# Kernel optimization log

Measured on AMD Instinct MI355X. Metric: run time of the kernel, lower is better.

## Reference

```python
import jax, jax.numpy as jnp
import numpy as np

D_MODEL = 5120
NUM_HEADS = 128
HEAD_DIM = D_MODEL // NUM_HEADS  # 40
LATENT = 1536


def setup_inputs() -> dict:
    key = jax.random.key(0)
    ks = jax.random.split(key, 9)
    B, S = 2, 1024
    scale = 0.02
    return {
        "x": jax.random.normal(ks[0], (B, S, D_MODEL), dtype=jnp.float32),
        "Wq": jax.random.normal(ks[1], (D_MODEL, D_MODEL), dtype=jnp.float32) * scale,
        "bq": jnp.zeros((D_MODEL,), dtype=jnp.float32),
        "Wc": jax.random.normal(ks[2], (D_MODEL, LATENT), dtype=jnp.float32) * scale,
        "bc": jnp.zeros((LATENT,), dtype=jnp.float32),
        "Wk": jax.random.normal(ks[3], (LATENT, D_MODEL), dtype=jnp.float32) * scale,
        "bk": jnp.zeros((D_MODEL,), dtype=jnp.float32),
        "Wv": jax.random.normal(ks[4], (LATENT, D_MODEL), dtype=jnp.float32) * scale,
        "bv": jnp.zeros((D_MODEL,), dtype=jnp.float32),
    }


def reference(x, Wq, bq, Wc, bc, Wk, bk, Wv, bv):
    B, S, _ = x.shape
    H, Dh = NUM_HEADS, HEAD_DIM
    # projections
    q = x @ Wq + bq                     # [B,S,D]
    kv_latent = x @ Wc + bc             # [B,S,L]
    k = kv_latent @ Wk + bk             # [B,S,D]
    v = kv_latent @ Wv + bv             # [B,S,D]
    # split heads -> [B,H,S,Dh]
    q = q.reshape(B, S, H, Dh).transpose(0, 2, 1, 3)
    k = k.reshape(B, S, H, Dh).transpose(0, 2, 1, 3)
    v = v.reshape(B, S, H, Dh).transpose(0, 2, 1, 3)
    scores = jnp.einsum("bhqd,bhkd->bhqk", q, k) / jnp.sqrt(jnp.float32(Dh))
    attn = jax.nn.softmax(scores, axis=-1)
    out = jnp.einsum("bhqk,bhkd->bhqd", attn, v)  # [B,H,S,Dh]
    return out.transpose(0, 2, 1, 3).reshape(B, S, H * Dh)
```

## Files before the change

kernel.cpp:

```cpp
#include <hip/hip_runtime.h>
#include <hip/hip_bf16.h>

typedef __attribute__((ext_vector_type(8))) __bf16 bf16x8;
typedef __attribute__((ext_vector_type(4))) __bf16 bf16x4;
typedef __attribute__((ext_vector_type(4))) float f32x4;

#define MFMA16(a, b, c) __builtin_amdgcn_mfma_f32_16x16x32_bf16((a), (b), (c), 0, 0, 0)

#if __has_builtin(__builtin_amdgcn_exp2f)
#define EXP2F(x) __builtin_amdgcn_exp2f(x)
#else
#define EXP2F(x) exp2f(x)
#endif

#define GLDS16(g, l)                                                             \
    __builtin_amdgcn_global_load_lds((const __attribute__((address_space(1))) void*)(g), \
                                     (__attribute__((address_space(3))) void*)(l), 16, 0, 0)

#define BARRIER()                          \
    do {                                   \
        asm volatile("" ::: "memory");     \
        __builtin_amdgcn_s_barrier();      \
        asm volatile("" ::: "memory");     \
    } while (0)

#define WAIT_LGKM0() asm volatile("s_waitcnt lgkmcnt(0)" ::: "memory")
#define VM6 asm volatile("s_waitcnt vmcnt(6)" ::: "memory")
#define VM8 asm volatile("s_waitcnt vmcnt(8)" ::: "memory")
#define VM0 asm volatile("s_waitcnt vmcnt(0)" ::: "memory")
#define VMNONE ((void)0)
#define KEEP(x) x
#define DROP(x)

static __device__ __forceinline__ unsigned short cvt_bf(float f) {
    return __builtin_bit_cast(unsigned short, (__bf16)f);
}

static __device__ __forceinline__ bf16x8 bf8_zero() {
    uint4 z = make_uint4(0, 0, 0, 0);
    return __builtin_bit_cast(bf16x8, z);
}

__global__ __launch_bounds__(256) void prep(const float* __restrict__ X,
                                            const float* __restrict__ Wq,
                                            const float* __restrict__ Wc,
                                            const float* __restrict__ Wk,
                                            const float* __restrict__ Wv,
                                            unsigned short* __restrict__ Xb,
                                            unsigned short* __restrict__ dqc,
                                            unsigned short* __restrict__ dkv) {
    const int D = 5120, L = 1536;
    int b = blockIdx.x, t = threadIdx.x;
    if (b < 5120) {
        int i = (b * 256 + t) * 8;
        float4 f0 = *(const float4*)(X + i);
        float4 f1 = *(const float4*)(X + i + 4);
        unsigned short o[8];
        o[0] = cvt_bf(f0.x); o[1] = cvt_bf(f0.y); o[2] = cvt_bf(f0.z); o[3] = cvt_bf(f0.w);
        o[4] = cvt_bf(f1.x); o[5] = cvt_bf(f1.y); o[6] = cvt_bf(f1.z); o[7] = cvt_bf(f1.w);
        *(uint4*)(Xb + i) = *(const uint4*)o;
        return;
    }
    int b2 = b - 5120;
    const float* W;
    unsigned short* WT;
    int K, N;
    if (b2 < 6400) { W = Wq; WT = dqc; K = D; N = D; }
    else if (b2 < 8320) { b2 -= 6400; W = Wc; WT = dqc + (size_t)D * D; K = D; N = L; }
    else if (b2 < 10240) { b2 -= 8320; W = Wk; WT = dkv; K = L; N = D; }
    else { b2 -= 10240; W = Wv; WT = dkv + (size_t)D * L; K = L; N = D; }
    int nx = N / 64;
    int n0 = (b2 % nx) * 64, k0 = (b2 / nx) * 64;

    __shared__ unsigned short tile[64][65];
    int c4 = (t & 15) * 4, r16 = t >> 4;
#pragma unroll
    for (int it = 0; it < 4; ++it) {
        int r = r16 + it * 16;
        float4 f = *(const float4*)&W[(size_t)(k0 + r) * N + n0 + c4];
        tile[r][c4 + 0] = cvt_bf(f.x);
        tile[r][c4 + 1] = cvt_bf(f.y);
        tile[r][c4 + 2] = cvt_bf(f.z);
        tile[r][c4 + 3] = cvt_bf(f.w);
    }
    __syncthreads();
    int n = t >> 2, kc = (t & 3) * 16;
    unsigned short o[16];
#pragma unroll
    for (int j = 0; j < 16; ++j) o[j] = tile[kc + j][n];
    unsigned short* dst = &WT[(size_t)(n0 + n) * K + k0 + kc];
    *(uint4*)dst = *(const uint4*)o;
    *(uint4*)(dst + 8) = *(const uint4*)(o + 8);
}

#define STAGE_A(S, H, KT)                                                              \
    do {                                                                               \
        GLDS16(aS[H][0] + (size_t)(KT) * 64, &Abuf[S][(H) * 8192 + wid * 512]);        \
        GLDS16(aS[H][1] + (size_t)(KT) * 64, &Abuf[S][(H) * 8192 + 4096 + wid * 512]); \
    } while (0)
#define STAGE_B(S, H, KT)                                                              \
    do {                                                                               \
        GLDS16(bS[H][0] + (size_t)(KT) * 64, &Bbuf[S][(H) * 8192 + wid * 512]);        \
        GLDS16(bS[H][1] + (size_t)(KT) * 64, &Bbuf[S][(H) * 8192 + 4096 + wid * 512]); \
    } while (0)

#define LDA_HALF(S, QM)                                                                   \
    do {                                                                                  \
        _Pragma("unroll") for (int mi = 0; mi < 4; ++mi)                                  \
            _Pragma("unroll") for (int kh = 0; kh < 2; ++kh)                              \
                af[mi][kh] =                                                              \
                    *(const bf16x8*)&Abuf[S][((QM) * 8192 + aoff + mi * 1024) ^ (kh * 32)]; \
    } while (0)
#define LDB_HALF(S, QN, BF)                                                               \
    do {                                                                                  \
        _Pragma("unroll") for (int ni = 0; ni < 2; ++ni)                                  \
            _Pragma("unroll") for (int kh = 0; kh < 2; ++kh)                              \
                BF[ni][kh] =                                                              \
                    *(const bf16x8*)&Bbuf[S][((QN) * 8192 + boff + ni * 1024) ^ (kh * 32)]; \
    } while (0)

#define MMAQ(QM, QN, BF)                                                                \
    do {                                                                                \
        _Pragma("unroll") for (int mi = 0; mi < 4; ++mi)                                \
            _Pragma("unroll") for (int ni = 0; ni < 2; ++ni)                            \
                _Pragma("unroll") for (int kh = 0; kh < 2; ++kh)                        \
                    acc[(QM) * 4 + mi][(QN) * 2 + ni] =                                 \
                        MFMA16(af[mi][kh], BF[ni][kh], acc[(QM) * 4 + mi][(QN) * 2 + ni]); \
    } while (0)

#define KTILE_V2(S, T, STG1, STG2, VMOP, RDNEXT)       \
    {                                                  \
        const int s_ = (S);                            \
        LDB_HALF(s_, 1, bf1);                          \
        STG1(STAGE_B(s_ ^ 1, 0, (T) + 1);)             \
        __builtin_amdgcn_s_setprio(1);                 \
        MMAQ(0, 0, bf0);                               \
        __builtin_amdgcn_s_setprio(0);                 \
        WAIT_LGKM0();                                  \
        BARRIER();                                     \
        STG2(STAGE_A(s_, 0, (T) + 2);                  \
             STAGE_B(s_, 1, (T) + 2);)                 \
        __builtin_amdgcn_s_setprio(1);                 \
        MMAQ(0, 1, bf1);                               \
        __builtin_amdgcn_s_setprio(0);                 \
        LDA_HALF(s_, 1);                               \
        __builtin_amdgcn_s_setprio(1);                 \
        MMAQ(1, 1, bf1);                               \
        __builtin_amdgcn_s_setprio(0);                 \
        WAIT_LGKM0();                                  \
        BARRIER();                                     \
        STG2(STAGE_A(s_, 1, (T) + 2);)                 \
        __builtin_amdgcn_s_setprio(1);                 \
        MMAQ(1, 0, bf0);                               \
        __builtin_amdgcn_s_setprio(0);                 \
        VMOP;                                          \
        BARRIER();                                     \
        RDNEXT(LDA_HALF(s_ ^ 1, 0); LDB_HALF(s_ ^ 1, 0, bf0);) \
    }

__global__ __launch_bounds__(512, 2) void gemm256(const unsigned short* __restrict__ A, int lda,
                                                  const unsigned short* __restrict__ BT, int ldb,
                                                  const float* __restrict__ bias0,
                                                  const float* __restrict__ bias1, int nsplit,
                                                  unsigned short* __restrict__ C, int ldc,
                                                  int K, float s0, float s1, int gx) {
    __shared__ __align__(16) unsigned short Abuf[2][16384];
    __shared__ __align__(16) unsigned short Bbuf[2][16384];

    int nwg = gridDim.x, orig = blockIdx.x;
    int cpx = nwg >> 3;
    int wgid = (orig & 7) * cpx + (orig >> 3);
    int tm = wgid / gx, tn = wgid % gx;
    int m0 = tm * 256, n0 = tn * 256;

    int tid = threadIdx.x, lane = tid & 63, wid = tid >> 6;
    int wm = wid >> 2, wn = wid & 3;
    int lrow = lane & 15, lkg = lane >> 4;

    int t5 = tid >> 3;
    int cole = ((tid & 7) ^ ((tid >> 3) & 7)) << 3;
    const unsigned short* aS[2][2];
    const unsigned short* bS[2][2];
#pragma unroll
    for (int H = 0; H < 2; ++H)
#pragma unroll
        for (int c = 0; c < 2; ++c) {
            int rA = (c << 7) | (H << 6) | t5;
            int rB = (((c << 1) | (t5 >> 5)) << 6) | (H << 5) | (t5 & 31);
            aS[H][c] = A + (size_t)(m0 + rA) * lda + cole;
            bS[H][c] = BT + (size_t)(n0 + rB) * ldb + cole;
        }

    int xorc = (lkg * 8) ^ ((lrow & 7) << 3);
    int aoff = wm * 4096 + lrow * 64 + xorc;
    int boff = wn * 2048 + lrow * 64 + xorc;

    f32x4 acc[8][4];
#pragma unroll
    for (int i = 0; i < 8; ++i)
#pragma unroll
        for (int j = 0; j < 4; ++j) acc[i][j] = (f32x4){0.f, 0.f, 0.f, 0.f};
    bf16x8 af[4][2], bf0[2][2], bf1[2][2];

    const int nkt = K >> 6;

    STAGE_A(0, 0, 0); STAGE_A(0, 1, 0); STAGE_B(0, 0, 0); STAGE_B(0, 1, 0);
    STAGE_A(1, 0, 1); STAGE_B(1, 1, 1); STAGE_A(1, 1, 1);
    VM6;
    BARRIER();
    LDA_HALF(0, 0);
    LDB_HALF(0, 0, bf0);

    int t = 0;
    for (; t + 2 < nkt; ++t) KTILE_V2(t & 1, t, KEEP, KEEP, VM6, KEEP);
    KTILE_V2(t & 1, t, KEEP, DROP, VM0, KEEP);
    ++t;
    KTILE_V2(t & 1, t, DROP, DROP, VMNONE, DROP);

#pragma unroll
    for (int ni = 0; ni < 4; ++ni) {
        int col = n0 + wn * 64 + ni * 16 + lrow;
        float bval = (col < nsplit) ? bias0[col] : bias1[col - nsplit];
        float scl = (col < nsplit) ? s0 : s1;
#pragma unroll
        for (int mi = 0; mi < 8; ++mi) {
            int row = m0 + wm * 128 + mi * 16 + lkg * 4;
#pragma unroll
            for (int j = 0; j < 4; ++j)
                C[(size_t)(row + j) * ldc + col] = cvt_bf((acc[mi][ni][j] + bval) * scl);
        }
    }
}

#define STG128(S, KT)                                                                  \
    do {                                                                               \
        _Pragma("unroll") for (int i_ = 0; i_ < 4; ++i_)                               \
            GLDS16(Ag + (size_t)(i_ * 32) * lda + (size_t)(KT) * 64,                   \
                   &Abuf[S][i_ * 2048 + wid * 512]);                                   \
        _Pragma("unroll") for (int i_ = 0; i_ < 4; ++i_)                               \
            GLDS16(Bg + (size_t)(i_ * 32) * ldb + (size_t)(KT) * 64,                   \
                   &Bbuf[S][i_ * 2048 + wid * 512]);                                   \
    } while (0)

__global__ __launch_bounds__(256, 4) void gemm128(const unsigned short* __restrict__ A, int lda,
                                                  const unsigned short* __restrict__ BT, int ldb,
                                                  const float* __restrict__ bias0,
                                                  const float* __restrict__ bias1, int nsplit,
                                                  unsigned short* __restrict__ C, int ldc,
                                                  int K, float s0, float s1, int gy) {
    __shared__ __align__(16) unsigned short Abuf[2][8192];
    __shared__ __align__(16) unsigned short Bbuf[2][8192];

    int b = blockIdx.x;
    int tm = b % gy, tn = b / gy;
    int m0 = tm * 128, n0 = tn * 128;
    int tid = threadIdx.x, lane = tid & 63, wid = tid >> 6;
    int wm = wid >> 1, wn = wid & 1;
    int lrow = lane & 15, lkg = lane >> 4;

    int srow = tid >> 3;
    int cole = ((tid & 7) ^ ((tid >> 3) & 7)) << 3;
    const unsigned short* Ag = A + (size_t)(m0 + srow) * lda + cole;
    const unsigned short* Bg = BT + (size_t)(n0 + srow) * ldb + cole;

    int xorc8 = (lrow & 7) << 3;
    int aoff = (wm * 64 + lrow) * 64;
    int boff = (wn * 64 + lrow) * 64;

    f32x4 acc[4][4];
#pragma unroll
    for (int i = 0; i < 4; ++i)
#pragma unroll
        for (int j = 0; j < 4; ++j) acc[i][j] = (f32x4){0.f, 0.f, 0.f, 0.f};

    const int nkt = K >> 6;
    STG128(0, 0);
    for (int t = 0; t < nkt; ++t) {
        const int cur = t & 1;
        if (t + 1 < nkt) {
            STG128(cur ^ 1, t + 1);
            VM8;
        } else {
            VM0;
        }
        BARRIER();
        bf16x8 af[4][2], bv[4][2];
#pragma unroll
        for (int mi = 0; mi < 4; ++mi)
#pragma unroll
            for (int kh = 0; kh < 2; ++kh)
                af[mi][kh] = *(const bf16x8*)&Abuf[cur][aoff + mi * 1024 + (((kh * 4 + lkg) << 3) ^ xorc8)];
#pragma unroll
        for (int ni = 0; ni < 4; ++ni)
#pragma unroll
            for (int kh = 0; kh < 2; ++kh)
                bv[ni][kh] = *(const bf16x8*)&Bbuf[cur][boff + ni * 1024 + (((kh * 4 + lkg) << 3) ^ xorc8)];
        __builtin_amdgcn_s_setprio(1);
#pragma unroll
        for (int mi = 0; mi < 4; ++mi)
#pragma unroll
            for (int ni = 0; ni < 4; ++ni)
#pragma unroll
                for (int kh = 0; kh < 2; ++kh)
                    acc[mi][ni] = MFMA16(af[mi][kh], bv[ni][kh], acc[mi][ni]);
        __builtin_amdgcn_s_setprio(0);
        BARRIER();
    }

#pragma unroll
    for (int ni = 0; ni < 4; ++ni) {
        int col = n0 + wn * 64 + ni * 16 + lrow;
        float bval = (col < nsplit) ? bias0[col] : bias1[col - nsplit];
        float scl = (col < nsplit) ? s0 : s1;
#pragma unroll
        for (int mi = 0; mi < 4; ++mi) {
            int row = m0 + wm * 64 + mi * 16 + lkg * 4;
#pragma unroll
            for (int j = 0; j < 4; ++j)
                C[(size_t)(row + j) * ldc + col] = cvt_bf((acc[mi][ni][j] + bval) * scl);
        }
    }
}

__global__ __launch_bounds__(256) void attn(const unsigned short* __restrict__ q, int ldq,
                                            const unsigned short* __restrict__ k, int ldk,
                                            const unsigned short* __restrict__ v, int ldv,
                                            float* __restrict__ out) {
    const int S = 1024, D = 5120, Dh = 40;
    int b = blockIdx.z, h = blockIdx.y, qt = blockIdx.x;
    int t = threadIdx.x, lane = t & 63, wid = t >> 6;
    int lrow = lane & 15, lkg = lane >> 4;

    __shared__ __align__(16) unsigned short Ks[64 * 72];
    __shared__ __align__(16) unsigned short Vs[64 * 72];
    __shared__ __align__(16) unsigned short Ps[4][16 * 72];

    const size_t qbase = ((size_t)b * S) * ldq + (size_t)h * Dh;
    int q0 = qt * 64 + wid * 16;

    bf16x8 qf0, qf1;
    {
        const unsigned short* qp = q + qbase + (size_t)(q0 + lrow) * ldq;
        qf0 = *(const bf16x8*)(qp + lkg * 8);
        qf1 = (lkg == 0) ? *(const bf16x8*)(qp + 32) : bf8_zero();
    }

    int rrK = t >> 3, ccK = t & 7;
    int rrV = t & 63, ccV = t >> 6;
    const unsigned short* kp = k + ((size_t)b * S) * ldk + (size_t)h * Dh +
                               (size_t)rrK * ldk + ccK * 8;
    const unsigned short* vp = v + ((size_t)b * S) * ldv + (size_t)h * Dh +
                               (size_t)rrV * ldv + ccV * 8;
    const size_t kstep = (size_t)64 * ldk, vstep = (size_t)64 * ldv;

    uint4 kv0, kv1, vv0, vv1;
    kv0 = kv1 = vv0 = vv1 = make_uint4(0, 0, 0, 0);
    if (ccK < 5) { kv0 = *(const uint4*)kp; kv1 = *(const uint4*)(kp + 32 * ldk); }
    vv0 = *(const uint4*)vp;
    if (ccV == 0) vv1 = *(const uint4*)(vp + 32);
    kp += kstep; vp += vstep;

    f32x4 acc[3];
#pragma unroll
    for (int nb = 0; nb < 3; ++nb) acc[nb] = (f32x4){0.f, 0.f, 0.f, 0.f};
    float mrun = -INFINITY, lrun = 0.f;

    for (int kt = 0; kt < 16; ++kt) {
        __syncthreads();
        uint4 w0 = (ccK < 5) ? kv0 : make_uint4(0, 0, 0, 0);
        uint4 w1 = (ccK < 5) ? kv1 : make_uint4(0, 0, 0, 0);
        *(uint4*)&Ks[rrK * 72 + ccK * 8] = w0;
        *(uint4*)&Ks[(rrK + 32) * 72 + ccK * 8] = w1;
        {
            const unsigned short* pv = (const unsigned short*)&vv0;
#pragma unroll
            for (int j = 0; j < 8; ++j) Vs[(ccV * 8 + j) * 72 + rrV] = pv[j];
            if (ccV < 2) {
                uint4 z = (ccV == 0) ? vv1 : make_uint4(0, 0, 0, 0);
                const unsigned short* pz = (const unsigned short*)&z;
#pragma unroll
                for (int j = 0; j < 8; ++j) Vs[((ccV + 4) * 8 + j) * 72 + rrV] = pz[j];
            }
        }
        __syncthreads();
        if (kt + 1 < 16) {
            if (ccK < 5) { kv0 = *(const uint4*)kp; kv1 = *(const uint4*)(kp + 32 * ldk); }
            vv0 = *(const uint4*)vp;
            if (ccV == 0) vv1 = *(const uint4*)(vp + 32);
            kp += kstep; vp += vstep;
        }

        f32x4 sf[4];
        __builtin_amdgcn_s_setprio(1);
#pragma unroll
        for (int nb = 0; nb < 4; ++nb) {
            sf[nb] = (f32x4){0.f, 0.f, 0.f, 0.f};
            bf16x8 kf0 = *(const bf16x8*)&Ks[(nb * 16 + lrow) * 72 + lkg * 8];
            bf16x8 kf1 = *(const bf16x8*)&Ks[(nb * 16 + lrow) * 72 + 32 + lkg * 8];
            sf[nb] = MFMA16(kf0, qf0, sf[nb]);
            sf[nb] = MFMA16(kf1, qf1, sf[nb]);
        }
        __builtin_amdgcn_s_setprio(0);

        float tm = sf[0][0];
#pragma unroll
        for (int nb = 0; nb < 4; ++nb)
#pragma unroll
            for (int i = 0; i < 4; ++i) tm = fmaxf(tm, sf[nb][i]);
        tm = fmaxf(tm, __shfl_xor(tm, 16));
        tm = fmaxf(tm, __shfl_xor(tm, 32));

        float mn = mrun, al = 1.0f;
        bool resc = !__all(tm <= mrun + 11.0f);
        if (resc) {
            mn = fmaxf(mrun, tm);
            al = EXP2F(mrun - mn);
            mrun = mn;
        }
        float rs = 0.f;
#pragma unroll
        for (int nb = 0; nb < 4; ++nb) {
            bf16x4 pk;
#pragma unroll
            for (int i = 0; i < 4; ++i) {
                float p = EXP2F(sf[nb][i] - mn);
                rs += p;
                pk[i] = (__bf16)p;
            }
            *(bf16x4*)&Ps[wid][lrow * 72 + nb * 16 + lkg * 4] = pk;
        }
        rs += __shfl_xor(rs, 16);
        rs += __shfl_xor(rs, 32);
        lrun = lrun * al + rs;

        if (resc) {
            float alr[4];
#pragma unroll
            for (int i = 0; i < 4; ++i) alr[i] = __shfl(al, lkg * 4 + i);
#pragma unroll
            for (int nb = 0; nb < 3; ++nb)
#pragma unroll
                for (int i = 0; i < 4; ++i) acc[nb][i] *= alr[i];
        }

        __builtin_amdgcn_s_setprio(1);
#pragma unroll
        for (int kk = 0; kk < 2; ++kk) {
            bf16x8 pf = *(const bf16x8*)&Ps[wid][lrow * 72 + kk * 32 + lkg * 8];
#pragma unroll
            for (int nb = 0; nb < 3; ++nb) {
                bf16x8 vf = *(const bf16x8*)&Vs[(nb * 16 + lrow) * 72 + kk * 32 + lkg * 8];
                acc[nb] = MFMA16(pf, vf, acc[nb]);
            }
        }
        __builtin_amdgcn_s_setprio(0);
    }

    float lr[4];
#pragma unroll
    for (int i = 0; i < 4; ++i) lr[i] = __shfl(lrun, lkg * 4 + i);
#pragma unroll
    for (int i = 0; i < 4; ++i) {
        float inv = 1.0f / lr[i];
        int s = q0 + lkg * 4 + i;
#pragma unroll
        for (int nb = 0; nb < 3; ++nb) {
            int d = nb * 16 + lrow;
            if (d < Dh) out[((size_t)(b * S + s)) * D + h * Dh + d] = acc[nb][i] * inv;
        }
    }
}

extern "C" void kernel_launch(void* const* d_in, const int* in_sizes, int n_in,
                              void* d_out, int out_size, void* d_ws, size_t ws_size,
                              hipStream_t stream) {
    const int M = 2048, D = 5120, L = 1536, NQ = D + L , NKV = 2 * D ;
    const float* x  = (const float*)d_in[0];
    const float* Wq = (const float*)d_in[1];
    const float* bq = (const float*)d_in[2];
    const float* Wc = (const float*)d_in[3];
    const float* bc = (const float*)d_in[4];
    const float* Wk = (const float*)d_in[5];
    const float* bk = (const float*)d_in[6];
    const float* Wv = (const float*)d_in[7];
    const float* bv = (const float*)d_in[8];
    float* out = (float*)d_out;

    unsigned short* ws = (unsigned short*)d_ws;
    size_t off = 0;
    unsigned short* xb    = ws + off; off += (size_t)M * D;
    unsigned short* WqcT  = ws + off; off += (size_t)NQ * D;
    unsigned short* WkvT  = ws + off; off += (size_t)NKV * L;
    unsigned short* qkvb  = ws + off; off += (size_t)M * NQ;
    unsigned short* kvout = ws + off; off += (size_t)M * NKV;

    prep<<<17280, 256, 0, stream>>>(x, Wq, Wc, Wk, Wv, xb, WqcT, WkvT);

    const float qscale = 1.4426950408889634f / 6.324555320336759f;

    gemm256<<<dim3((NQ / 256) * (M / 256)), 512, 0, stream>>>(xb, D, WqcT, D, bq, bc, D,
                                                              qkvb, NQ, D, qscale, 1.0f,
                                                              NQ / 256);
    gemm128<<<dim3((NKV / 128) * (M / 128)), 256, 0, stream>>>(qkvb + D, NQ, WkvT, L, bk, bv, D,
                                                               kvout, NKV, L, 1.0f, 1.0f,
                                                               M / 128);

    attn<<<dim3(1024 / 64, 128, 2), 256, 0, stream>>>(qkvb, NQ, kvout, NKV, kvout + D, NKV, out);
}
```

Before: 466.0 us.

## Load GEMM B operand directly to registers and pre-transpose V for attention

The KV-projection GEMM now stages only the A tile through LDS and loads B fragments straight from global memory into registers, double-buffered two k-tiles ahead. This cuts LDS traffic and halves LDS use per block. A new vtrans kernel transposes V into a [D, tokens] buffer so the attention kernel can write V tiles to shared memory with vector stores instead of scalar scatter-transposes. The cost is an extra kernel launch plus a full round trip of V through memory, and B loads that now run uncoalesced across lanes.

```diff
diff --git a/kernel.cpp b/kernel.cpp
--- a/kernel.cpp
+++ b/kernel.cpp
@@ -26,7 +26,7 @@
 
 #define WAIT_LGKM0() asm volatile("s_waitcnt lgkmcnt(0)" ::: "memory")
 #define VM6 asm volatile("s_waitcnt vmcnt(6)" ::: "memory")
-#define VM8 asm volatile("s_waitcnt vmcnt(8)" ::: "memory")
+#define VM12 asm volatile("s_waitcnt vmcnt(12)" ::: "memory")
 #define VM0 asm volatile("s_waitcnt vmcnt(0)" ::: "memory")
 #define VMNONE ((void)0)
 #define KEEP(x) x
@@ -91,6 +91,28 @@
     unsigned short* dst = &WT[(size_t)(n0 + n) * K + k0 + kc];
     *(uint4*)dst = *(const uint4*)o;
     *(uint4*)(dst + 8) = *(const uint4*)(o + 8);
+}
+
+__global__ __launch_bounds__(256) void vtrans(const unsigned short* __restrict__ V, int ldv,
+                                              unsigned short* __restrict__ VT) {
+    int d0 = blockIdx.x * 64, s0 = blockIdx.y * 64;
+    __shared__ __align__(16) unsigned short tile[64][72];
+    int t = threadIdx.x;
+    int r = t >> 3, c8 = (t & 7) * 8;
+#pragma unroll
+    for (int p = 0; p < 2; ++p) {
+        uint4 u = *(const uint4*)&V[(size_t)(s0 + r + p * 32) * ldv + d0 + c8];
+        *(uint4*)&tile[r + p * 32][c8] = u;
+    }
+    __syncthreads();
+#pragma unroll
+    for (int p = 0; p < 2; ++p) {
+        int dr = (t >> 3) + p * 32, cc = (t & 7) * 8;
+        unsigned short o[8];
+#pragma unroll
+        for (int j = 0; j < 8; ++j) o[j] = tile[cc + j][dr];
+        *(uint4*)&VT[(size_t)(d0 + dr) * 2048 + s0 + cc] = *(const uint4*)o;
+    }
 }
 
 #define STAGE_A(S, H, KT)                                                              \
@@ -232,24 +254,46 @@
     }
 }
 
-#define STG128(S, KT)                                                                  \
+#define STGA128(P, T)                                                                  \
     do {                                                                               \
         _Pragma("unroll") for (int i_ = 0; i_ < 4; ++i_)                               \
-            GLDS16(Ag + (size_t)(i_ * 32) * lda + (size_t)(KT) * 64,                   \
-                   &Abuf[S][i_ * 2048 + wid * 512]);                                   \
-        _Pragma("unroll") for (int i_ = 0; i_ < 4; ++i_)                               \
-            GLDS16(Bg + (size_t)(i_ * 32) * ldb + (size_t)(KT) * 64,                   \
-                   &Bbuf[S][i_ * 2048 + wid * 512]);                                   \
-    } while (0)
-
-__global__ __launch_bounds__(256, 4) void gemm128(const unsigned short* __restrict__ A, int lda,
-                                                  const unsigned short* __restrict__ BT, int ldb,
-                                                  const float* __restrict__ bias0,
-                                                  const float* __restrict__ bias1, int nsplit,
-                                                  unsigned short* __restrict__ C, int ldc,
-                                                  int K, float s0, float s1, int gy) {
+            GLDS16(Ag + (size_t)(i_ * 32) * lda + (size_t)(T) * 64,                    \
+                   &Abuf[P][i_ * 2048 + wid * 512]);                                   \
+    } while (0)
+#define LDBQ(BV, T)                                                                    \
+    do {                                                                               \
+        _Pragma("unroll") for (int ni = 0; ni < 4; ++ni)                               \
+            _Pragma("unroll") for (int kh = 0; kh < 2; ++kh)                           \
+                BV[ni][kh] = *(const bf16x8*)(Bg[ni] + (size_t)(T) * 64 + kh * 32);    \
+    } while (0)
+
+#define ITERB(BV, P, T, STG_, LDB2_, VMOP)                                             \
+    {                                                                                  \
+        STG_(STGA128((P) ^ 1, (T) + 1);)                                               \
+        VMOP;                                                                          \
+        BARRIER();                                                                     \
+        bf16x8 af[4][2];                                                               \
+        _Pragma("unroll") for (int mi = 0; mi < 4; ++mi)                               \
+            _Pragma("unroll") for (int kh = 0; kh < 2; ++kh)                           \
+                af[mi][kh] = *(const bf16x8*)&Abuf[P][aoff + mi * 1024 +               \
+                                                      (((kh * 4 + lkg) << 3) ^ xorc8)]; \
+        __builtin_amdgcn_s_setprio(1);                                                 \
+        _Pragma("unroll") for (int mi = 0; mi < 4; ++mi)                               \
+            _Pragma("unroll") for (int ni = 0; ni < 4; ++ni)                           \
+                _Pragma("unroll") for (int kh = 0; kh < 2; ++kh)                       \
+                    acc[mi][ni] = MFMA16(af[mi][kh], BV[ni][kh], acc[mi][ni]);         \
+        __builtin_amdgcn_s_setprio(0);                                                 \
+        LDB2_(LDBQ(BV, (T) + 2);)                                                      \
+        BARRIER();                                                                     \
+    }
+
+__global__ __launch_bounds__(256, 4) void gemm128b(const unsigned short* __restrict__ A, int lda,
+                                                   const unsigned short* __restrict__ BT, int ldb,
+                                                   const float* __restrict__ bias0,
+                                                   const float* __restrict__ bias1, int nsplit,
+                                                   unsigned short* __restrict__ C, int ldc,
+                                                   int K, int gy) {
     __shared__ __align__(16) unsigned short Abuf[2][8192];
-    __shared__ __align__(16) unsigned short Bbuf[2][8192];
 
     int b = blockIdx.x;
     int tm = b % gy, tn = b / gy;
@@ -261,70 +305,52 @@
     int srow = tid >> 3;
     int cole = ((tid & 7) ^ ((tid >> 3) & 7)) << 3;
     const unsigned short* Ag = A + (size_t)(m0 + srow) * lda + cole;
-    const unsigned short* Bg = BT + (size_t)(n0 + srow) * ldb + cole;
+    const unsigned short* Bg[4];
+#pragma unroll
+    for (int ni = 0; ni < 4; ++ni)
+        Bg[ni] = BT + (size_t)(n0 + wn * 64 + ni * 16 + lrow) * ldb + lkg * 8;
 
     int xorc8 = (lrow & 7) << 3;
     int aoff = (wm * 64 + lrow) * 64;
-    int boff = (wn * 64 + lrow) * 64;
 
     f32x4 acc[4][4];
 #pragma unroll
     for (int i = 0; i < 4; ++i)
 #pragma unroll
         for (int j = 0; j < 4; ++j) acc[i][j] = (f32x4){0.f, 0.f, 0.f, 0.f};
+    bf16x8 bv0[4][2], bv1[4][2];
 
     const int nkt = K >> 6;
-    STG128(0, 0);
-    for (int t = 0; t < nkt; ++t) {
-        const int cur = t & 1;
-        if (t + 1 < nkt) {
-            STG128(cur ^ 1, t + 1);
-            VM8;
-        } else {
-            VM0;
-        }
-        BARRIER();
-        bf16x8 af[4][2], bv[4][2];
-#pragma unroll
-        for (int mi = 0; mi < 4; ++mi)
-#pragma unroll
-            for (int kh = 0; kh < 2; ++kh)
-                af[mi][kh] = *(const bf16x8*)&Abuf[cur][aoff + mi * 1024 + (((kh * 4 + lkg) << 3) ^ xorc8)];
-#pragma unroll
-        for (int ni = 0; ni < 4; ++ni)
-#pragma unroll
-            for (int kh = 0; kh < 2; ++kh)
-                bv[ni][kh] = *(const bf16x8*)&Bbuf[cur][boff + ni * 1024 + (((kh * 4 + lkg) << 3) ^ xorc8)];
-        __builtin_amdgcn_s_setprio(1);
-#pragma unroll
-        for (int mi = 0; mi < 4; ++mi)
-#pragma unroll
-            for (int ni = 0; ni < 4; ++ni)
-#pragma unroll
-                for (int kh = 0; kh < 2; ++kh)
-                    acc[mi][ni] = MFMA16(af[mi][kh], bv[ni][kh], acc[mi][ni]);
-        __builtin_amdgcn_s_setprio(0);
-        BARRIER();
-    }
+
+    LDBQ(bv0, 0);
+    STGA128(0, 0);
+    LDBQ(bv1, 1);
+
+    int T = 0;
+    for (; T + 2 < nkt; T += 2) {
+        ITERB(bv0, 0, T, KEEP, KEEP, VM12);
+        ITERB(bv1, 1, T + 1, KEEP, KEEP, VM12);
+    }
+    ITERB(bv0, 0, T, KEEP, DROP, VM12);
+    ITERB(bv1, 1, T + 1, DROP, DROP, VM0);
 
 #pragma unroll
     for (int ni = 0; ni < 4; ++ni) {
         int col = n0 + wn * 64 + ni * 16 + lrow;
         float bval = (col < nsplit) ? bias0[col] : bias1[col - nsplit];
-        float scl = (col < nsplit) ? s0 : s1;
 #pragma unroll
         for (int mi = 0; mi < 4; ++mi) {
             int row = m0 + wm * 64 + mi * 16 + lkg * 4;
 #pragma unroll
             for (int j = 0; j < 4; ++j)
-                C[(size_t)(row + j) * ldc + col] = cvt_bf((acc[mi][ni][j] + bval) * scl);
+                C[(size_t)(row + j) * ldc + col] = cvt_bf(acc[mi][ni][j] + bval);
         }
     }
 }
 
 __global__ __launch_bounds__(256) void attn(const unsigned short* __restrict__ q, int ldq,
                                             const unsigned short* __restrict__ k, int ldk,
-                                            const unsigned short* __restrict__ v, int ldv,
+                                            const unsigned short* __restrict__ vT,
                                             float* __restrict__ out) {
     const int S = 1024, D = 5120, Dh = 40;
     int b = blockIdx.z, h = blockIdx.y, qt = blockIdx.x;
@@ -332,11 +358,13 @@
     int lrow = lane & 15, lkg = lane >> 4;
 
     __shared__ __align__(16) unsigned short Ks[64 * 72];
-    __shared__ __align__(16) unsigned short Vs[64 * 72];
+    __shared__ __align__(16) unsigned short Vs[48 * 72];
     __shared__ __align__(16) unsigned short Ps[4][16 * 72];
 
     const size_t qbase = ((size_t)b * S) * ldq + (size_t)h * Dh;
     int q0 = qt * 64 + wid * 16;
+
+    for (int z = t; z < 8 * 72; z += 256) Vs[40 * 72 + z] = 0;
 
     bf16x8 qf0, qf1;
     {
@@ -346,19 +374,19 @@
     }
 
     int rrK = t >> 3, ccK = t & 7;
-    int rrV = t & 63, ccV = t >> 6;
+    int dV = t >> 3, cV = t & 7;
     const unsigned short* kp = k + ((size_t)b * S) * ldk + (size_t)h * Dh +
                                (size_t)rrK * ldk + ccK * 8;
-    const unsigned short* vp = v + ((size_t)b * S) * ldv + (size_t)h * Dh +
-                               (size_t)rrV * ldv + ccV * 8;
-    const size_t kstep = (size_t)64 * ldk, vstep = (size_t)64 * ldv;
-
-    uint4 kv0, kv1, vv0, vv1;
-    kv0 = kv1 = vv0 = vv1 = make_uint4(0, 0, 0, 0);
+    const unsigned short* vp = vT + (size_t)(h * Dh + dV) * 2048 + b * S + cV * 8;
+    const unsigned short* vp2 = vT + (size_t)(h * Dh + 32 + dV) * 2048 + b * S + cV * 8;
+    const size_t kstep = (size_t)64 * ldk;
+
+    uint4 kv0, kv1, va0, va1;
+    kv0 = kv1 = va0 = va1 = make_uint4(0, 0, 0, 0);
     if (ccK < 5) { kv0 = *(const uint4*)kp; kv1 = *(const uint4*)(kp + 32 * ldk); }
-    vv0 = *(const uint4*)vp;
-    if (ccV == 0) vv1 = *(const uint4*)(vp + 32);
-    kp += kstep; vp += vstep;
+    va0 = *(const uint4*)vp;
+    if (t < 64) va1 = *(const uint4*)vp2;
+    kp += kstep; vp += 64; vp2 += 64;
 
     f32x4 acc[3];
 #pragma unroll
@@ -371,23 +399,14 @@
         uint4 w1 = (ccK < 5) ? kv1 : make_uint4(0, 0, 0, 0);
         *(uint4*)&Ks[rrK * 72 + ccK * 8] = w0;
         *(uint4*)&Ks[(rrK + 32) * 72 + ccK * 8] = w1;
-        {
-            const unsigned short* pv = (const unsigned short*)&vv0;
-#pragma unroll
-            for (int j = 0; j < 8; ++j) Vs[(ccV * 8 + j) * 72 + rrV] = pv[j];
-            if (ccV < 2) {
-                uint4 z = (ccV == 0) ? vv1 : make_uint4(0, 0, 0, 0);
-                const unsigned short* pz = (const unsigned short*)&z;
-#pragma unroll
-                for (int j = 0; j < 8; ++j) Vs[((ccV + 4) * 8 + j) * 72 + rrV] = pz[j];
-            }
-        }
+        *(uint4*)&Vs[dV * 72 + cV * 8] = va0;
+        if (t < 64) *(uint4*)&Vs[(32 + dV) * 72 + cV * 8] = va1;
         __syncthreads();
         if (kt + 1 < 16) {
             if (ccK < 5) { kv0 = *(const uint4*)kp; kv1 = *(const uint4*)(kp + 32 * ldk); }
-            vv0 = *(const uint4*)vp;
-            if (ccV == 0) vv1 = *(const uint4*)(vp + 32);
-            kp += kstep; vp += vstep;
+            va0 = *(const uint4*)vp;
+            if (t < 64) va1 = *(const uint4*)vp2;
+            kp += kstep; vp += 64; vp2 += 64;
         }
 
         f32x4 sf[4];
@@ -493,6 +512,7 @@
     unsigned short* WkvT  = ws + off; off += (size_t)NKV * L;
     unsigned short* qkvb  = ws + off; off += (size_t)M * NQ;
     unsigned short* kvout = ws + off; off += (size_t)M * NKV;
+    unsigned short* vTb   = ws + off; off += (size_t)D * M;
 
     prep<<<17280, 256, 0, stream>>>(x, Wq, Wc, Wk, Wv, xb, WqcT, WkvT);
 
@@ -501,9 +521,9 @@
     gemm256<<<dim3((NQ / 256) * (M / 256)), 512, 0, stream>>>(xb, D, WqcT, D, bq, bc, D,
                                                               qkvb, NQ, D, qscale, 1.0f,
                                                               NQ / 256);
-    gemm128<<<dim3((NKV / 128) * (M / 128)), 256, 0, stream>>>(qkvb + D, NQ, WkvT, L, bk, bv, D,
-                                                               kvout, NKV, L, 1.0f, 1.0f,
-                                                               M / 128);
-
-    attn<<<dim3(1024 / 64, 128, 2), 256, 0, stream>>>(qkvb, NQ, kvout, NKV, kvout + D, NKV, out);
-}
+    gemm128b<<<dim3((NKV / 128) * (M / 128)), 256, 0, stream>>>(qkvb + D, NQ, WkvT, L, bk, bv,
+                                                                D, kvout, NKV, L, M / 128);
+    vtrans<<<dim3(D / 64, M / 64), 256, 0, stream>>>(kvout + D, NKV, vTb);
+
+    attn<<<dim3(1024 / 64, 128, 2), 256, 0, stream>>>(qkvb, NQ, kvout, NKV, vTb, out);
+}
```

After: 1.089 ms. 2.34x slower.

## Pre-transpose V into a separate buffer so attention loads it with vector stores

Applied to the files above, without the earlier changes.

Adds a vtrans kernel that writes V in a [D, tokens] transposed layout. The attention kernel can then fill its V shared tile with 16-byte vector writes instead of scattered 2-byte transposed stores, and the padding rows are zeroed once up front. This costs an extra kernel launch plus a full read and write of V through global memory. The gemm128 launch bound is also relaxed from 4 to 2 waves per SIMD, giving the compiler more register room at the risk of lower occupancy.

```diff
diff --git a/kernel.cpp b/kernel.cpp
--- a/kernel.cpp
+++ b/kernel.cpp
@@ -91,6 +91,28 @@
     unsigned short* dst = &WT[(size_t)(n0 + n) * K + k0 + kc];
     *(uint4*)dst = *(const uint4*)o;
     *(uint4*)(dst + 8) = *(const uint4*)(o + 8);
+}
+
+__global__ __launch_bounds__(256) void vtrans(const unsigned short* __restrict__ V, int ldv,
+                                              unsigned short* __restrict__ VT) {
+    int d0 = blockIdx.x * 64, s0 = blockIdx.y * 64;
+    __shared__ __align__(16) unsigned short tile[64][72];
+    int t = threadIdx.x;
+    int r = t >> 3, c8 = (t & 7) * 8;
+#pragma unroll
+    for (int p = 0; p < 2; ++p) {
+        uint4 u = *(const uint4*)&V[(size_t)(s0 + r + p * 32) * ldv + d0 + c8];
+        *(uint4*)&tile[r + p * 32][c8] = u;
+    }
+    __syncthreads();
+#pragma unroll
+    for (int p = 0; p < 2; ++p) {
+        int dr = (t >> 3) + p * 32, cc = (t & 7) * 8;
+        unsigned short o[8];
+#pragma unroll
+        for (int j = 0; j < 8; ++j) o[j] = tile[cc + j][dr];
+        *(uint4*)&VT[(size_t)(d0 + dr) * 2048 + s0 + cc] = *(const uint4*)o;
+    }
 }
 
 #define STAGE_A(S, H, KT)                                                              \
@@ -242,7 +264,7 @@
                    &Bbuf[S][i_ * 2048 + wid * 512]);                                   \
     } while (0)
 
-__global__ __launch_bounds__(256, 4) void gemm128(const unsigned short* __restrict__ A, int lda,
+__global__ __launch_bounds__(256, 2) void gemm128(const unsigned short* __restrict__ A, int lda,
                                                   const unsigned short* __restrict__ BT, int ldb,
                                                   const float* __restrict__ bias0,
                                                   const float* __restrict__ bias1, int nsplit,
@@ -269,9 +291,9 @@
 
     f32x4 acc[4][4];
 #pragma unroll
-    for (int i = 0; i < 4; ++i)
-#pragma unroll
-        for (int j = 0; j < 4; ++j) acc[i][j] = (f32x4){0.f, 0.f, 0.f, 0.f};
+    for (int i2 = 0; i2 < 4; ++i2)
+#pragma unroll
+        for (int j = 0; j < 4; ++j) acc[i2][j] = (f32x4){0.f, 0.f, 0.f, 0.f};
 
     const int nkt = K >> 6;
     STG128(0, 0);
@@ -324,7 +346,7 @@
 
 __global__ __launch_bounds__(256) void attn(const unsigned short* __restrict__ q, int ldq,
                                             const unsigned short* __restrict__ k, int ldk,
-                                            const unsigned short* __restrict__ v, int ldv,
+                                            const unsigned short* __restrict__ vT,
                                             float* __restrict__ out) {
     const int S = 1024, D = 5120, Dh = 40;
     int b = blockIdx.z, h = blockIdx.y, qt = blockIdx.x;
@@ -332,11 +354,13 @@
     int lrow = lane & 15, lkg = lane >> 4;
 
     __shared__ __align__(16) unsigned short Ks[64 * 72];
-    __shared__ __align__(16) unsigned short Vs[64 * 72];
+    __shared__ __align__(16) unsigned short Vs[48 * 72];
     __shared__ __align__(16) unsigned short Ps[4][16 * 72];
 
     const size_t qbase = ((size_t)b * S) * ldq + (size_t)h * Dh;
     int q0 = qt * 64 + wid * 16;
+
+    for (int z = t; z < 8 * 72; z += 256) Vs[40 * 72 + z] = 0;
 
     bf16x8 qf0, qf1;
     {
@@ -346,19 +370,19 @@
     }
 
     int rrK = t >> 3, ccK = t & 7;
-    int rrV = t & 63, ccV = t >> 6;
+    int dV = t >> 3, cV = t & 7;
     const unsigned short* kp = k + ((size_t)b * S) * ldk + (size_t)h * Dh +
                                (size_t)rrK * ldk + ccK * 8;
-    const unsigned short* vp = v + ((size_t)b * S) * ldv + (size_t)h * Dh +
-                               (size_t)rrV * ldv + ccV * 8;
-    const size_t kstep = (size_t)64 * ldk, vstep = (size_t)64 * ldv;
-
-    uint4 kv0, kv1, vv0, vv1;
-    kv0 = kv1 = vv0 = vv1 = make_uint4(0, 0, 0, 0);
+    const unsigned short* vp = vT + (size_t)(h * Dh + dV) * 2048 + b * S + cV * 8;
+    const unsigned short* vp2 = vT + (size_t)(h * Dh + 32 + dV) * 2048 + b * S + cV * 8;
+    const size_t kstep = (size_t)64 * ldk;
+
+    uint4 kv0, kv1, va0, va1;
+    kv0 = kv1 = va0 = va1 = make_uint4(0, 0, 0, 0);
     if (ccK < 5) { kv0 = *(const uint4*)kp; kv1 = *(const uint4*)(kp + 32 * ldk); }
-    vv0 = *(const uint4*)vp;
-    if (ccV == 0) vv1 = *(const uint4*)(vp + 32);
-    kp += kstep; vp += vstep;
+    va0 = *(const uint4*)vp;
+    if (t < 64) va1 = *(const uint4*)vp2;
+    kp += kstep; vp += 64; vp2 += 64;
 
     f32x4 acc[3];
 #pragma unroll
@@ -371,23 +395,14 @@
         uint4 w1 = (ccK < 5) ? kv1 : make_uint4(0, 0, 0, 0);
         *(uint4*)&Ks[rrK * 72 + ccK * 8] = w0;
         *(uint4*)&Ks[(rrK + 32) * 72 + ccK * 8] = w1;
-        {
-            const unsigned short* pv = (const unsigned short*)&vv0;
-#pragma unroll
-            for (int j = 0; j < 8; ++j) Vs[(ccV * 8 + j) * 72 + rrV] = pv[j];
-            if (ccV < 2) {
-                uint4 z = (ccV == 0) ? vv1 : make_uint4(0, 0, 0, 0);
-                const unsigned short* pz = (const unsigned short*)&z;
-#pragma unroll
-                for (int j = 0; j < 8; ++j) Vs[((ccV + 4) * 8 + j) * 72 + rrV] = pz[j];
-            }
-        }
+        *(uint4*)&Vs[dV * 72 + cV * 8] = va0;
+        if (t < 64) *(uint4*)&Vs[(32 + dV) * 72 + cV * 8] = va1;
         __syncthreads();
         if (kt + 1 < 16) {
             if (ccK < 5) { kv0 = *(const uint4*)kp; kv1 = *(const uint4*)(kp + 32 * ldk); }
-            vv0 = *(const uint4*)vp;
-            if (ccV == 0) vv1 = *(const uint4*)(vp + 32);
-            kp += kstep; vp += vstep;
+            va0 = *(const uint4*)vp;
+            if (t < 64) va1 = *(const uint4*)vp2;
+            kp += kstep; vp += 64; vp2 += 64;
         }
 
         f32x4 sf[4];
@@ -493,6 +508,7 @@
     unsigned short* WkvT  = ws + off; off += (size_t)NKV * L;
     unsigned short* qkvb  = ws + off; off += (size_t)M * NQ;
     unsigned short* kvout = ws + off; off += (size_t)M * NKV;
+    unsigned short* vTb   = ws + off; off += (size_t)D * M;
 
     prep<<<17280, 256, 0, stream>>>(x, Wq, Wc, Wk, Wv, xb, WqcT, WkvT);
 
@@ -504,6 +520,7 @@
     gemm128<<<dim3((NKV / 128) * (M / 128)), 256, 0, stream>>>(qkvb + D, NQ, WkvT, L, bk, bv, D,
                                                                kvout, NKV, L, 1.0f, 1.0f,
                                                                M / 128);
-
-    attn<<<dim3(1024 / 64, 128, 2), 256, 0, stream>>>(qkvb, NQ, kvout, NKV, kvout + D, NKV, out);
-}
+    vtrans<<<dim3(D / 64, M / 64), 256, 0, stream>>>(kvout + D, NKV, vTb);
+
+    attn<<<dim3(1024 / 64, 128, 2), 256, 0, stream>>>(qkvb, NQ, kvout, NKV, vTb, out);
+}
```

Result: no change. 457.4 us (-1.8%).
